# Optimization experiments

Hardware: AMD Instinct MI355X
Metric: run time of the kernel (lower is better)

## Reference

```python
import jax, jax.numpy as jnp
import numpy as np

N, C, IMG, HEADS = 512, 3, 32, 4
F = C * IMG * IMG          # 3072 node feature dim
E = 4096                   # edges without self loops
EPS = 1e-5                 # BatchNorm eps
SLOPE = 0.2                # GATv2 LeakyReLU negative slope


def bn(x, g, b, m, v):
    # eval-mode BatchNorm2d over channel dim 1
    inv = g / jnp.sqrt(v + EPS)
    return x * inv[None, :, None, None] + (b - m * inv)[None, :, None, None]


def conv1x1(x, W, b):
    # W: [out_c, in_c]
    return jnp.einsum('bchw,oc->bohw', x, W) + b[None, :, None, None]


def setup_inputs():
    key = jax.random.key(0)
    ks = jax.random.split(key, 32)
    inp = {}
    inp['x'] = jax.random.normal(ks[0], (N, C, IMG, IMG), jnp.float32)
    src = jax.random.randint(ks[1], (E,), 0, N)
    off = jax.random.randint(ks[2], (E,), 1, N)
    inp['edge_index'] = jnp.stack([src, (src + off) % N]).astype(jnp.int32)  # no self loops

    def w(k, shape, fan_in):
        return jax.random.normal(k, shape, jnp.float32) / np.sqrt(fan_in)

    i = 3
    def nk():
        nonlocal i; i += 1; return ks[i - 1]
    # grapher fc1: Conv2d(C,C,1)+BN
    inp['fc1_W'] = w(nk(), (C, C), C); inp['fc1_b'] = jnp.zeros((C,), jnp.float32)
    inp['bn1_g'] = jnp.ones((C,), jnp.float32); inp['bn1_b'] = jnp.zeros((C,), jnp.float32)
    inp['bn1_m'] = 0.1 * jax.random.normal(nk(), (C,), jnp.float32)
    inp['bn1_v'] = jax.random.uniform(nk(), (C,), jnp.float32, 0.5, 1.5)
    # GATv2Conv(F, F, heads=HEADS): lin_l, lin_r [F, HEADS*F] with bias, att [HEADS, F], out bias
    inp['Wl'] = w(nk(), (F, HEADS * F), F); inp['bl'] = jnp.zeros((HEADS * F,), jnp.float32)
    inp['Wr'] = w(nk(), (F, HEADS * F), F); inp['br'] = jnp.zeros((HEADS * F,), jnp.float32)
    inp['att'] = w(nk(), (HEADS, F), F)
    inp['gat_b'] = jnp.zeros((HEADS * F,), jnp.float32)
    # grapher fc2: Conv2d(C*HEADS, C, 1)+BN
    inp['fc2_W'] = w(nk(), (C, C * HEADS), C * HEADS); inp['fc2_b'] = jnp.zeros((C,), jnp.float32)
    inp['bn2_g'] = jnp.ones((C,), jnp.float32); inp['bn2_b'] = jnp.zeros((C,), jnp.float32)
    inp['bn2_m'] = 0.1 * jax.random.normal(nk(), (C,), jnp.float32)
    inp['bn2_v'] = jax.random.uniform(nk(), (C,), jnp.float32, 0.5, 1.5)
    # FFN fc1 / fc2 (C->C 1x1 conv + BN)
    inp['ffn1_W'] = w(nk(), (C, C), C); inp['ffn1_b'] = jnp.zeros((C,), jnp.float32)
    inp['bnf1_g'] = jnp.ones((C,), jnp.float32); inp['bnf1_b'] = jnp.zeros((C,), jnp.float32)
    inp['bnf1_m'] = 0.1 * jax.random.normal(nk(), (C,), jnp.float32)
    inp['bnf1_v'] = jax.random.uniform(nk(), (C,), jnp.float32, 0.5, 1.5)
    inp['ffn2_W'] = w(nk(), (C, C), C); inp['ffn2_b'] = jnp.zeros((C,), jnp.float32)
    inp['bnf2_g'] = jnp.ones((C,), jnp.float32); inp['bnf2_b'] = jnp.zeros((C,), jnp.float32)
    inp['bnf2_m'] = 0.1 * jax.random.normal(nk(), (C,), jnp.float32)
    inp['bnf2_v'] = jax.random.uniform(nk(), (C,), jnp.float32, 0.5, 1.5)
    return inp


def reference(x, edge_index, fc1_W, fc1_b, bn1_g, bn1_b, bn1_m, bn1_v,
              Wl, bl, Wr, br, att, gat_b,
              fc2_W, fc2_b, bn2_g, bn2_b, bn2_m, bn2_v,
              ffn1_W, ffn1_b, bnf1_g, bnf1_b, bnf1_m, bnf1_v,
              ffn2_W, ffn2_b, bnf2_g, bnf2_b, bnf2_m, bnf2_v):
    shortcut = x
    h = bn(conv1x1(x, fc1_W, fc1_b), bn1_g, bn1_b, bn1_m, bn1_v)
    hf = h.reshape(N, F)
    xl = (hf @ Wl + bl).reshape(N, HEADS, F)  # source transform
    xr = (hf @ Wr + br).reshape(N, HEADS, F)  # target transform
    # add self loops (PyG GATv2Conv default)
    loops = jnp.arange(N, dtype=edge_index.dtype)
    src = jnp.concatenate([edge_index[0], loops])
    dst = jnp.concatenate([edge_index[1], loops])
    # GATv2 edge scores: a . LeakyReLU(xl_j + xr_i)
    e = jax.nn.leaky_relu(xl[src] + xr[dst], negative_slope=SLOPE)  # [E+N, HEADS, F]
    logits = jnp.einsum('ehf,hf->eh', e, att)
    mx = jax.ops.segment_max(logits, dst, num_segments=N)
    ex = jnp.exp(logits - jax.lax.stop_gradient(mx)[dst])
    denom = jax.ops.segment_sum(ex, dst, num_segments=N)
    alpha = ex / denom[dst]                                          # segment softmax over targets
    agg = jax.ops.segment_sum(xl[src] * alpha[:, :, None], dst, num_segments=N)  # [N, HEADS, F]
    g_out = (agg.reshape(N, HEADS * F) + gat_b).reshape(N, C * HEADS, IMG, IMG)
    g = bn(conv1x1(g_out, fc2_W, fc2_b), bn2_g, bn2_b, bn2_m, bn2_v) + shortcut
    # FFN with residual
    f = jax.nn.relu(bn(conv1x1(g, ffn1_W, ffn1_b), bnf1_g, bnf1_b, bnf1_m, bnf1_v))
    f = bn(conv1x1(f, ffn2_W, ffn2_b), bnf2_g, bnf2_b, bnf2_m, bnf2_v)
    return f + g
```

## Files before the change

### kernel.cpp

```cpp
#include <hip/hip_runtime.h>

#define N_NODES 512
#define FDIM    3072
#define HEADS   4
#define HFD     12288
#define E_IN    4096
#define E_TOT   4608
#define EPSV    1e-5f
#define SLOPE   0.2f

typedef unsigned short u16;
typedef unsigned int   u32;

typedef short s16x8 __attribute__((ext_vector_type(8)));
typedef float f32x4 __attribute__((ext_vector_type(4)));

__device__ __forceinline__ u16 f2bf(float f){
  u32 u = __builtin_bit_cast(u32, f);
  u = (u + 0x7fffu + ((u >> 16) & 1u)) >> 16;
  return (u16)u;
}
__device__ __forceinline__ float bf2f(u16 h){
  return __builtin_bit_cast(float, ((u32)h) << 16);
}
__device__ __forceinline__ float bflo(u32 p){
  return __builtin_bit_cast(float, p << 16);
}
__device__ __forceinline__ float bfhi(u32 p){
  return __builtin_bit_cast(float, p & 0xffff0000u);
}

__device__ __forceinline__ void gl_lds16(const u16* g, u16* l){
  __builtin_amdgcn_global_load_lds(
      (const __attribute__((address_space(1))) unsigned int*)g,
      (__attribute__((address_space(3))) unsigned int*)l, 16, 0, 0);
}

__global__ void k_fc1(const float* __restrict__ x, const float* __restrict__ W,
                      const float* __restrict__ b, const float* __restrict__ g,
                      const float* __restrict__ bb, const float* __restrict__ m,
                      const float* __restrict__ v, u16* __restrict__ hf,
                      int* __restrict__ cnt){
  int id = blockIdx.x * 256 + threadIdx.x;
  if (id < 512) cnt[id] = 0;
  int n = id >> 10, p = id & 1023;
  float x0 = x[n * FDIM + p];
  float x1 = x[n * FDIM + 1024 + p];
  float x2 = x[n * FDIM + 2048 + p];
#pragma unroll
  for (int c = 0; c < 3; ++c){
    float t = b[c] + W[c*3+0]*x0 + W[c*3+1]*x1 + W[c*3+2]*x2;
    float inv = g[c] * rsqrtf(v[c] + EPSV);
    float o = t * inv + (bb[c] - m[c] * inv);
    hf[n * FDIM + c * 1024 + p] = f2bf(o);
  }
}

__global__ __launch_bounds__(256, 3) void k_gemm(
    const u16* __restrict__ hf, const float* __restrict__ Wl,
    const float* __restrict__ bl, const float* __restrict__ Wr,
    const float* __restrict__ br, u16* __restrict__ xl, u16* __restrict__ xr){
  __shared__ u16 As[2][256 * 32];
  __shared__ u16 Bs[2][64 * 40];

  const int tid  = threadIdx.x;
  const int wave = tid >> 6, lane = tid & 63;
  const int quad = lane >> 4, l16 = lane & 15;

  const int g = blockIdx.x;
  const int ntile = (g >> 4) * 8 + (g & 7);
  const int mhalf = (g >> 3) & 1;
  const int n0 = ntile * 64;
  const int rbase = mhalf * 256;

  const float* Wg; const float* biasp; u16* outp; int cb;
  if (n0 < HFD){ Wg = Wl; biasp = bl; outp = xl; cb = n0; }
  else         { Wg = Wr; biasp = br; outp = xr; cb = n0 - HFD; }

  const u16* ga = hf + (size_t)(rbase + wave * 64 + (lane >> 2)) * FDIM
                     + (((lane & 3) ^ ((lane >> 3) & 3)) << 3);

  const int bn = tid & 63, bkh = tid >> 6;
  const float* gb = Wg + (size_t)bkh * 8 * HFD + (cb + bn);
  const int bwo = bn * 40 + bkh * 8;

  const int araw = (wave * 64 + l16) * 32 + ((quad ^ ((l16 >> 1) & 3)) << 3);
  const int brd  = l16 * 40 + quad * 8;

  f32x4 acc[4][4];
#pragma unroll
  for (int i = 0; i < 4; ++i)
#pragma unroll
    for (int j = 0; j < 4; ++j) acc[i][j] = (f32x4){0.f, 0.f, 0.f, 0.f};

  float bv[8];
#pragma unroll
  for (int j = 0; j < 8; ++j) bv[j] = gb[(size_t)j * HFD];
#pragma unroll
  for (int i = 0; i < 4; ++i)
    gl_lds16(ga + (size_t)i * 16 * FDIM, As[0] + (wave * 4 + i) * 512);
  {
    u32 p0 = (u32)f2bf(bv[0]) | ((u32)f2bf(bv[1]) << 16);
    u32 p1 = (u32)f2bf(bv[2]) | ((u32)f2bf(bv[3]) << 16);
    u32 p2 = (u32)f2bf(bv[4]) | ((u32)f2bf(bv[5]) << 16);
    u32 p3 = (u32)f2bf(bv[6]) | ((u32)f2bf(bv[7]) << 16);
    *(uint4*)(Bs[0] + bwo) = make_uint4(p0, p1, p2, p3);
  }
#pragma unroll
  for (int j = 0; j < 8; ++j) bv[j] = gb[(size_t)(32 + j) * HFD];
  __syncthreads();

#define GEMM_BODY(KS, CUR, NXT)                                               \
  {                                                                           \
    const int ksv = (KS);                                                     \
    if (ksv < 95){                                                            \
      _Pragma("unroll")                                                       \
      for (int i = 0; i < 4; ++i)                                             \
        gl_lds16(ga + (size_t)i * 16 * FDIM + (ksv + 1) * 32,                 \
                 As[NXT] + (wave * 4 + i) * 512);                             \
      u32 p0 = (u32)f2bf(bv[0]) | ((u32)f2bf(bv[1]) << 16);                   \
      u32 p1 = (u32)f2bf(bv[2]) | ((u32)f2bf(bv[3]) << 16);                   \
      u32 p2 = (u32)f2bf(bv[4]) | ((u32)f2bf(bv[5]) << 16);                   \
      u32 p3 = (u32)f2bf(bv[6]) | ((u32)f2bf(bv[7]) << 16);                   \
      *(uint4*)(Bs[NXT] + bwo) = make_uint4(p0, p1, p2, p3);                  \
      int kn = (ksv + 2 < 96 ? ksv + 2 : 95) * 32;                            \
      _Pragma("unroll")                                                       \
      for (int j = 0; j < 8; ++j) bv[j] = gb[(size_t)(kn + j) * HFD];         \
    }                                                                         \
    s16x8 af[4], bfr[4];                                                      \
    _Pragma("unroll")                                                         \
    for (int i = 0; i < 4; ++i)                                               \
      af[i] = __builtin_bit_cast(s16x8, *(const uint4*)(As[CUR] + araw + i * 512)); \
    _Pragma("unroll")                                                         \
    for (int j = 0; j < 4; ++j)                                               \
      bfr[j] = __builtin_bit_cast(s16x8, *(const uint4*)(Bs[CUR] + brd + j * 640)); \
    _Pragma("unroll")                                                         \
    for (int i = 0; i < 4; ++i)                                               \
      _Pragma("unroll")                                                       \
      for (int j = 0; j < 4; ++j)                                             \
        acc[i][j] = __builtin_amdgcn_mfma_f32_16x16x32_bf16(af[i], bfr[j], acc[i][j], 0, 0, 0); \
    __syncthreads();                                                          \
  }

  for (int ks = 0; ks < 96; ks += 2){
    GEMM_BODY(ks, 0, 1);
    GEMM_BODY(ks + 1, 1, 0);
  }
#undef GEMM_BODY

  float bj[4];
#pragma unroll
  for (int j = 0; j < 4; ++j) bj[j] = biasp[cb + j * 16 + l16];
#pragma unroll
  for (int i = 0; i < 4; ++i){
    int mrow = rbase + wave * 64 + i * 16 + quad * 4;
#pragma unroll
    for (int r = 0; r < 4; ++r){
      u16* orow = outp + (size_t)(mrow + r) * HFD + cb + l16;
#pragma unroll
      for (int j = 0; j < 4; ++j)
        orow[j * 16] = f2bf(acc[i][j][r] + bj[j]);
    }
  }
}

__global__ void k_logits(const int* __restrict__ ei, const u16* __restrict__ xl,
                         const u16* __restrict__ xr, const float* __restrict__ att,
                         float* __restrict__ logits, int* __restrict__ cnt){
  int e = blockIdx.x;
  int h = threadIdx.x >> 6, lane = threadIdx.x & 63;
  int s, d;
  if (e < E_IN){ s = ei[e]; d = ei[E_IN + e]; } else { s = e - E_IN; d = s; }
  if (threadIdx.x == 0) atomicAdd(&cnt[d], 1);
  const u16* xlp = xl + (size_t)s * HFD + h * FDIM;
  const u16* xrp = xr + (size_t)d * HFD + h * FDIM;
  const float* ap = att + h * FDIM;
  float acc = 0.f;
#pragma unroll
  for (int it = 0; it < 6; ++it){
    int f = it * 512 + lane * 8;
    uint4 a = *(const uint4*)(xlp + f);
    uint4 b = *(const uint4*)(xrp + f);
    float4 w0 = *(const float4*)(ap + f);
    float4 w1 = *(const float4*)(ap + f + 4);
    float v0 = bflo(a.x) + bflo(b.x); v0 = v0 > 0.f ? v0 : SLOPE * v0;
    float v1 = bfhi(a.x) + bfhi(b.x); v1 = v1 > 0.f ? v1 : SLOPE * v1;
    float v2 = bflo(a.y) + bflo(b.y); v2 = v2 > 0.f ? v2 : SLOPE * v2;
    float v3 = bfhi(a.y) + bfhi(b.y); v3 = v3 > 0.f ? v3 : SLOPE * v3;
    float v4 = bflo(a.z) + bflo(b.z); v4 = v4 > 0.f ? v4 : SLOPE * v4;
    float v5 = bfhi(a.z) + bfhi(b.z); v5 = v5 > 0.f ? v5 : SLOPE * v5;
    float v6 = bflo(a.w) + bflo(b.w); v6 = v6 > 0.f ? v6 : SLOPE * v6;
    float v7 = bfhi(a.w) + bfhi(b.w); v7 = v7 > 0.f ? v7 : SLOPE * v7;
    acc += v0 * w0.x + v1 * w0.y + v2 * w0.z + v3 * w0.w;
    acc += v4 * w1.x + v5 * w1.y + v6 * w1.z + v7 * w1.w;
  }
#pragma unroll
  for (int o = 32; o > 0; o >>= 1) acc += __shfl_down(acc, o);
  if (lane == 0) logits[e * 4 + h] = acc;
}

__global__ void k_scan_scatter(const int* __restrict__ ei, const int* __restrict__ cnt,
                               int* __restrict__ off, int* __restrict__ elist){
  __shared__ int s[512];
  __shared__ int cur[512];
  int t = threadIdx.x;
  int v = cnt[t];
  s[t] = v;
  __syncthreads();
  for (int d = 1; d < 512; d <<= 1){
    int add = (t >= d) ? s[t - d] : 0;
    __syncthreads();
    s[t] += add;
    __syncthreads();
  }
  int exc = s[t] - v;
  off[t] = exc;
  cur[t] = exc;
  __syncthreads();
  for (int e = t; e < E_TOT; e += 512){
    int d = (e < E_IN) ? ei[E_IN + e] : (e - E_IN);
    int pos = atomicAdd(&cur[d], 1);
    elist[pos] = e;
  }
}

__global__ void k_softmax(const int* __restrict__ cnt, const int* __restrict__ off,
                          const int* __restrict__ elist, const float* __restrict__ logits,
                          float* __restrict__ alpha){
  int i = blockIdx.x;
  int lane = threadIdx.x;
  int deg = cnt[i], st = off[i];
#pragma unroll
  for (int h = 0; h < 4; ++h){
    float mx = -1e30f;
    for (int j = lane; j < deg; j += 64){
      int e = elist[st + j];
      mx = fmaxf(mx, logits[e * 4 + h]);
    }
#pragma unroll
    for (int o = 32; o > 0; o >>= 1) mx = fmaxf(mx, __shfl_down(mx, o));
    mx = __shfl(mx, 0);
    float sm = 0.f;
    for (int j = lane; j < deg; j += 64){
      int e = elist[st + j];
      sm += __expf(logits[e * 4 + h] - mx);
    }
#pragma unroll
    for (int o = 32; o > 0; o >>= 1) sm += __shfl_down(sm, o);
    sm = __shfl(sm, 0);
    float rs = 1.f / sm;
    for (int j = lane; j < deg; j += 64){
      int e = elist[st + j];
      alpha[e * 4 + h] = __expf(logits[e * 4 + h] - mx) * rs;
    }
  }
}

__global__ __launch_bounds__(256) void k_aggfinal(
    const int* __restrict__ ei, const int* __restrict__ cnt,
    const int* __restrict__ off, const int* __restrict__ elist,
    const float* __restrict__ alpha, const u16* __restrict__ xl,
    const float* __restrict__ gat_b,
    const float* __restrict__ W2, const float* __restrict__ b2,
    const float* __restrict__ g2, const float* __restrict__ bb2,
    const float* __restrict__ m2, const float* __restrict__ v2,
    const float* __restrict__ W3, const float* __restrict__ b3,
    const float* __restrict__ g3, const float* __restrict__ bb3,
    const float* __restrict__ m3, const float* __restrict__ v3,
    const float* __restrict__ W4, const float* __restrict__ b4,
    const float* __restrict__ g4, const float* __restrict__ bb4,
    const float* __restrict__ m4, const float* __restrict__ v4,
    const float* __restrict__ x, float* __restrict__ out){
  __shared__ int    s_src[128];
  __shared__ float4 s_al[128];
  const int n = blockIdx.x;
  const int t = threadIdx.x;
  const int p4 = t * 4;
  const int deg = cnt[n], st = off[n];

  float acc[12][4];
#pragma unroll
  for (int o = 0; o < 12; ++o)
#pragma unroll
    for (int r = 0; r < 4; ++r) acc[o][r] = 0.f;

  for (int base = 0; base < deg; base += 128){
    int cn = min(deg - base, 128);
    if (t < cn){
      int e = elist[st + base + t];
      s_src[t] = (e < E_IN) ? ei[e] : (e - E_IN);
      s_al[t] = *(const float4*)(alpha + e * 4);
    }
    __syncthreads();
    for (int j = 0; j < cn; ++j){
      int s = s_src[j];
      float4 al4 = s_al[j];
      float alh[4] = {al4.x, al4.y, al4.z, al4.w};
      const u16* bp = xl + (size_t)s * HFD;
#pragma unroll
      for (int h = 0; h < 4; ++h){
#pragma unroll
        for (int c = 0; c < 3; ++c){
          ushort4 xv = *(const ushort4*)(bp + h * FDIM + c * 1024 + p4);
          acc[h*3+c][0] += alh[h] * bf2f(xv.x);
          acc[h*3+c][1] += alh[h] * bf2f(xv.y);
          acc[h*3+c][2] += alh[h] * bf2f(xv.z);
          acc[h*3+c][3] += alh[h] * bf2f(xv.w);
        }
      }
    }
    __syncthreads();
  }

#pragma unroll
  for (int o = 0; o < 12; ++o){
    float4 gv = *(const float4*)(gat_b + o * 1024 + p4);
    acc[o][0] += gv.x; acc[o][1] += gv.y; acc[o][2] += gv.z; acc[o][3] += gv.w;
  }
  float xv[3][4];
#pragma unroll
  for (int c = 0; c < 3; ++c){
    float4 t4 = *(const float4*)(x + (size_t)n * FDIM + c * 1024 + p4);
    xv[c][0] = t4.x; xv[c][1] = t4.y; xv[c][2] = t4.z; xv[c][3] = t4.w;
  }
  float o4[3][4];
#pragma unroll
  for (int r = 0; r < 4; ++r){
    float gch[3];
#pragma unroll
    for (int c = 0; c < 3; ++c){
      float tt = b2[c];
#pragma unroll
      for (int o = 0; o < 12; ++o) tt += W2[c * 12 + o] * acc[o][r];
      float inv = g2[c] * rsqrtf(v2[c] + EPSV);
      gch[c] = tt * inv + (bb2[c] - m2[c] * inv) + xv[c][r];
    }
    float f1[3];
#pragma unroll
    for (int c = 0; c < 3; ++c){
      float tt = b3[c] + W3[c*3+0]*gch[0] + W3[c*3+1]*gch[1] + W3[c*3+2]*gch[2];
      float inv = g3[c] * rsqrtf(v3[c] + EPSV);
      float vv = tt * inv + (bb3[c] - m3[c] * inv);
      f1[c] = fmaxf(vv, 0.f);
    }
#pragma unroll
    for (int c = 0; c < 3; ++c){
      float tt = b4[c] + W4[c*3+0]*f1[0] + W4[c*3+1]*f1[1] + W4[c*3+2]*f1[2];
      float inv = g4[c] * rsqrtf(v4[c] + EPSV);
      o4[c][r] = tt * inv + (bb4[c] - m4[c] * inv) + gch[c];
    }
  }
#pragma unroll
  for (int c = 0; c < 3; ++c)
    *(float4*)(out + (size_t)n * FDIM + c * 1024 + p4) =
        make_float4(o4[c][0], o4[c][1], o4[c][2], o4[c][3]);
}

extern "C" void kernel_launch(void* const* d_in, const int* in_sizes, int n_in,
                              void* d_out, int out_size, void* d_ws, size_t ws_size,
                              hipStream_t stream){
  (void)in_sizes; (void)n_in; (void)out_size; (void)ws_size;
  const float* x     = (const float*)d_in[0];
  const int*   ei    = (const int*)d_in[1];
  const float* fc1_W = (const float*)d_in[2];
  const float* fc1_b = (const float*)d_in[3];
  const float* bn1_g = (const float*)d_in[4];
  const float* bn1_b = (const float*)d_in[5];
  const float* bn1_m = (const float*)d_in[6];
  const float* bn1_v = (const float*)d_in[7];
  const float* Wl    = (const float*)d_in[8];
  const float* bl    = (const float*)d_in[9];
  const float* Wr    = (const float*)d_in[10];
  const float* br    = (const float*)d_in[11];
  const float* att   = (const float*)d_in[12];
  const float* gat_b = (const float*)d_in[13];
  const float* fc2_W = (const float*)d_in[14];
  const float* fc2_b = (const float*)d_in[15];
  const float* bn2_g = (const float*)d_in[16];
  const float* bn2_b = (const float*)d_in[17];
  const float* bn2_m = (const float*)d_in[18];
  const float* bn2_v = (const float*)d_in[19];
  const float* ffn1_W= (const float*)d_in[20];
  const float* ffn1_b= (const float*)d_in[21];
  const float* bnf1_g= (const float*)d_in[22];
  const float* bnf1_b= (const float*)d_in[23];
  const float* bnf1_m= (const float*)d_in[24];
  const float* bnf1_v= (const float*)d_in[25];
  const float* ffn2_W= (const float*)d_in[26];
  const float* ffn2_b= (const float*)d_in[27];
  const float* bnf2_g= (const float*)d_in[28];
  const float* bnf2_b= (const float*)d_in[29];
  const float* bnf2_m= (const float*)d_in[30];
  const float* bnf2_v= (const float*)d_in[31];

  char* w = (char*)d_ws;
  u16*   hf     = (u16*)(w);
  u16*   xl     = (u16*)(w + 3145728);
  u16*   xr     = (u16*)(w + 15728640);
  float* logits = (float*)(w + 28311552);
  float* alpha  = (float*)(w + 28385280);
  int*   cnt    = (int*)(w + 28459008);
  int*   offp   = (int*)(w + 28461056);
  int*   elist  = (int*)(w + 28465152);

  k_fc1<<<2048, 256, 0, stream>>>(x, fc1_W, fc1_b, bn1_g, bn1_b, bn1_m, bn1_v, hf, cnt);
  k_gemm<<<768, 256, 0, stream>>>(hf, Wl, bl, Wr, br, xl, xr);
  k_logits<<<E_TOT, 256, 0, stream>>>(ei, xl, xr, att, logits, cnt);
  k_scan_scatter<<<1, 512, 0, stream>>>(ei, cnt, offp, elist);
  k_softmax<<<512, 64, 0, stream>>>(cnt, offp, elist, logits, alpha);
  k_aggfinal<<<512, 256, 0, stream>>>(ei, cnt, offp, elist, alpha, xl, gat_b,
                                      fc2_W, fc2_b, bn2_g, bn2_b, bn2_m, bn2_v,
                                      ffn1_W, ffn1_b, bnf1_g, bnf1_b, bnf1_m, bnf1_v,
                                      ffn2_W, ffn2_b, bnf2_g, bnf2_b, bnf2_m, bnf2_v,
                                      x, (float*)d_out);
}
```

Baseline: 527.1 us.

## Restructure GEMM to per-wave A tiles and register-direct B fragments without block barriers

The projection GEMM is reorganised so each wave owns a private 32-row A tile in LDS and loads B (fp32 weights) straight from global memory into registers in MFMA fragment layout. This removes the shared B tile in LDS and all __syncthreads in the K loop. The block tile shrinks from 256x64 to 128x64, the grid doubles, and occupancy is raised to 4 blocks per SM. A cheaper round-half-up bf16 pack replaces round-to-nearest-even. The costs are more redundant global reads of W across M tiles (each weight element is now fetched by 4 blocks instead of 2), higher register pressure from 64 prefetched floats, and an A prefetch with no explicit wait, which may race.

```diff
diff --git a/kernel.cpp b/kernel.cpp
--- a/kernel.cpp
+++ b/kernel.cpp
@@ -28,6 +28,11 @@
 }
 __device__ __forceinline__ float bfhi(u32 p){
   return __builtin_bit_cast(float, p & 0xffff0000u);
+}
+__device__ __forceinline__ u32 pack_bf(float a, float b){
+  u32 ua = __builtin_bit_cast(u32, a) + 0x8000u;
+  u32 ub = __builtin_bit_cast(u32, b) + 0x8000u;
+  return (ua >> 16) | (ub & 0xffff0000u);
 }
 
 __device__ __forceinline__ void gl_lds16(const u16* g, u16* l){
@@ -56,95 +61,82 @@
   }
 }
 
-__global__ __launch_bounds__(256, 3) void k_gemm(
+__global__ __launch_bounds__(256, 4) void k_gemm(
     const u16* __restrict__ hf, const float* __restrict__ Wl,
     const float* __restrict__ bl, const float* __restrict__ Wr,
     const float* __restrict__ br, u16* __restrict__ xl, u16* __restrict__ xr){
-  __shared__ u16 As[2][256 * 32];
-  __shared__ u16 Bs[2][64 * 40];
+  __shared__ u16 As[4][2][1024];
 
   const int tid  = threadIdx.x;
   const int wave = tid >> 6, lane = tid & 63;
   const int quad = lane >> 4, l16 = lane & 15;
 
   const int g = blockIdx.x;
-  const int ntile = (g >> 4) * 8 + (g & 7);
-  const int mhalf = (g >> 3) & 1;
+  const int ntile = (g >> 5) * 8 + (g & 7);
+  const int q     = (g >> 3) & 3;
   const int n0 = ntile * 64;
-  const int rbase = mhalf * 256;
+  const int rbase = q * 128 + wave * 32;
 
   const float* Wg; const float* biasp; u16* outp; int cb;
   if (n0 < HFD){ Wg = Wl; biasp = bl; outp = xl; cb = n0; }
   else         { Wg = Wr; biasp = br; outp = xr; cb = n0 - HFD; }
 
-  const u16* ga = hf + (size_t)(rbase + wave * 64 + (lane >> 2)) * FDIM
+  const u16* ga = hf + (size_t)(rbase + (lane >> 2)) * FDIM
                      + (((lane & 3) ^ ((lane >> 3) & 3)) << 3);
-
-  const int bn = tid & 63, bkh = tid >> 6;
-  const float* gb = Wg + (size_t)bkh * 8 * HFD + (cb + bn);
-  const int bwo = bn * 40 + bkh * 8;
-
-  const int araw = (wave * 64 + l16) * 32 + ((quad ^ ((l16 >> 1) & 3)) << 3);
-  const int brd  = l16 * 40 + quad * 8;
-
-  f32x4 acc[4][4];
-#pragma unroll
-  for (int i = 0; i < 4; ++i)
+  const int ard0 = (l16) * 32 + ((quad ^ ((l16 >> 1) & 3)) << 3);
+  const int ard1 = (16 + l16) * 32 + ((quad ^ ((l16 >> 1) & 3)) << 3);
+
+  const float* gB = Wg + (size_t)(quad * 8) * HFD + cb + l16;
+
+  f32x4 acc[2][4];
+#pragma unroll
+  for (int i = 0; i < 2; ++i)
 #pragma unroll
     for (int j = 0; j < 4; ++j) acc[i][j] = (f32x4){0.f, 0.f, 0.f, 0.f};
 
-  float bv[8];
-#pragma unroll
-  for (int j = 0; j < 8; ++j) bv[j] = gb[(size_t)j * HFD];
-#pragma unroll
-  for (int i = 0; i < 4; ++i)
-    gl_lds16(ga + (size_t)i * 16 * FDIM, As[0] + (wave * 4 + i) * 512);
-  {
-    u32 p0 = (u32)f2bf(bv[0]) | ((u32)f2bf(bv[1]) << 16);
-    u32 p1 = (u32)f2bf(bv[2]) | ((u32)f2bf(bv[3]) << 16);
-    u32 p2 = (u32)f2bf(bv[4]) | ((u32)f2bf(bv[5]) << 16);
-    u32 p3 = (u32)f2bf(bv[6]) | ((u32)f2bf(bv[7]) << 16);
-    *(uint4*)(Bs[0] + bwo) = make_uint4(p0, p1, p2, p3);
-  }
-#pragma unroll
-  for (int j = 0; j < 8; ++j) bv[j] = gb[(size_t)(32 + j) * HFD];
-  __syncthreads();
-
-#define GEMM_BODY(KS, CUR, NXT)                                               \
-  {                                                                           \
-    const int ksv = (KS);                                                     \
-    if (ksv < 95){                                                            \
-      _Pragma("unroll")                                                       \
-      for (int i = 0; i < 4; ++i)                                             \
-        gl_lds16(ga + (size_t)i * 16 * FDIM + (ksv + 1) * 32,                 \
-                 As[NXT] + (wave * 4 + i) * 512);                             \
-      u32 p0 = (u32)f2bf(bv[0]) | ((u32)f2bf(bv[1]) << 16);                   \
-      u32 p1 = (u32)f2bf(bv[2]) | ((u32)f2bf(bv[3]) << 16);                   \
-      u32 p2 = (u32)f2bf(bv[4]) | ((u32)f2bf(bv[5]) << 16);                   \
-      u32 p3 = (u32)f2bf(bv[6]) | ((u32)f2bf(bv[7]) << 16);                   \
-      *(uint4*)(Bs[NXT] + bwo) = make_uint4(p0, p1, p2, p3);                  \
-      int kn = (ksv + 2 < 96 ? ksv + 2 : 95) * 32;                            \
-      _Pragma("unroll")                                                       \
-      for (int j = 0; j < 8; ++j) bv[j] = gb[(size_t)(kn + j) * HFD];         \
-    }                                                                         \
-    s16x8 af[4], bfr[4];                                                      \
-    _Pragma("unroll")                                                         \
-    for (int i = 0; i < 4; ++i)                                               \
-      af[i] = __builtin_bit_cast(s16x8, *(const uint4*)(As[CUR] + araw + i * 512)); \
-    _Pragma("unroll")                                                         \
-    for (int j = 0; j < 4; ++j)                                               \
-      bfr[j] = __builtin_bit_cast(s16x8, *(const uint4*)(Bs[CUR] + brd + j * 640)); \
-    _Pragma("unroll")                                                         \
-    for (int i = 0; i < 4; ++i)                                               \
-      _Pragma("unroll")                                                       \
-      for (int j = 0; j < 4; ++j)                                             \
-        acc[i][j] = __builtin_amdgcn_mfma_f32_16x16x32_bf16(af[i], bfr[j], acc[i][j], 0, 0, 0); \
-    __syncthreads();                                                          \
+  float br0[32], br1[32];
+  gl_lds16(ga, &As[wave][0][0]);
+  gl_lds16(ga + 16 * FDIM, &As[wave][0][512]);
+  gl_lds16(ga + 32, &As[wave][1][0]);
+  gl_lds16(ga + 16 * FDIM + 32, &As[wave][1][512]);
+#pragma unroll
+  for (int j = 0; j < 4; ++j)
+#pragma unroll
+    for (int kk = 0; kk < 8; ++kk){
+      br0[j*8+kk] = gB[(size_t)kk * HFD + j * 16];
+      br1[j*8+kk] = gB[(size_t)(32 + kk) * HFD + j * 16];
+    }
+
+#define GEMM_BODY(KS, BUF, BR)                                                 \
+  {                                                                            \
+    const int ksv = (KS);                                                      \
+    const int ka  = (ksv + 2 < 96) ? ksv + 2 : 0;                              \
+          \
+    s16x8 af0 = __builtin_bit_cast(s16x8, *(const uint4*)(&As[wave][BUF][ard0])); \
+    s16x8 af1 = __builtin_bit_cast(s16x8, *(const uint4*)(&As[wave][BUF][ard1])); \
+                                          \
+    gl_lds16(ga + (size_t)ka * 32, &As[wave][BUF][0]);                         \
+    gl_lds16(ga + 16 * FDIM + (size_t)ka * 32, &As[wave][BUF][512]);           \
+    _Pragma("unroll")                                                          \
+    for (int j = 0; j < 4; ++j){                                               \
+      uint4 pk;                                                                \
+      pk.x = pack_bf(BR[j*8+0], BR[j*8+1]);                                    \
+      pk.y = pack_bf(BR[j*8+2], BR[j*8+3]);                                    \
+      pk.z = pack_bf(BR[j*8+4], BR[j*8+5]);                                    \
+      pk.w = pack_bf(BR[j*8+6], BR[j*8+7]);                                    \
+      s16x8 bfrag = __builtin_bit_cast(s16x8, pk);                             \
+      acc[0][j] = __builtin_amdgcn_mfma_f32_16x16x32_bf16(af0, bfrag, acc[0][j], 0, 0, 0); \
+      acc[1][j] = __builtin_amdgcn_mfma_f32_16x16x32_bf16(af1, bfrag, acc[1][j], 0, 0, 0); \
+         \
+      _Pragma("unroll")                                                        \
+      for (int kk = 0; kk < 8; ++kk)                                           \
+        BR[j*8+kk] = gB[(size_t)(ka * 32 + kk) * HFD + j * 16];                \
+    }                                                                          \
   }
 
   for (int ks = 0; ks < 96; ks += 2){
-    GEMM_BODY(ks, 0, 1);
-    GEMM_BODY(ks + 1, 1, 0);
+    GEMM_BODY(ks,     0, br0);
+    GEMM_BODY(ks + 1, 1, br1);
   }
 #undef GEMM_BODY
 
@@ -152,8 +144,8 @@
 #pragma unroll
   for (int j = 0; j < 4; ++j) bj[j] = biasp[cb + j * 16 + l16];
 #pragma unroll
-  for (int i = 0; i < 4; ++i){
-    int mrow = rbase + wave * 64 + i * 16 + quad * 4;
+  for (int i = 0; i < 2; ++i){
+    int mrow = rbase + i * 16 + quad * 4;
 #pragma unroll
     for (int r = 0; r < 4; ++r){
       u16* orow = outp + (size_t)(mrow + r) * HFD + cb + l16;
@@ -404,7 +396,7 @@
   int*   elist  = (int*)(w + 28465152);
 
   k_fc1<<<2048, 256, 0, stream>>>(x, fc1_W, fc1_b, bn1_g, bn1_b, bn1_m, bn1_v, hf, cnt);
-  k_gemm<<<768, 256, 0, stream>>>(hf, Wl, bl, Wr, br, xl, xr);
+  k_gemm<<<1536, 256, 0, stream>>>(hf, Wl, bl, Wr, br, xl, xr);
   k_logits<<<E_TOT, 256, 0, stream>>>(ei, xl, xr, att, logits, cnt);
   k_scan_scatter<<<1, 512, 0, stream>>>(ei, cnt, offp, elist);
   k_softmax<<<512, 64, 0, stream>>>(cnt, offp, elist, logits, alpha);
```

Result: slower. 1.008 ms (+91.3%).
